# Performance work log

Measured on AMD Instinct MI355X. Metric: run time of the kernel, lower is better.

The kernel has to match this reference:

```python
import jax, jax.numpy as jnp
import numpy as np

DIM = 199  # number of graph nodes, hardcoded in the source repo
K_HOP = 3


def _khop_support(n, k):
    # Ring graph adjacency with self loops, then k-hop reachability mask.
    A = np.eye(n, dtype=np.float64)
    idx = np.arange(n)
    A[idx, (idx + 1) % n] = 1.0
    A[(idx + 1) % n, idx] = 1.0
    S = np.linalg.matrix_power(A, k)
    return (S > 0).astype(np.float32)


def setup_inputs() -> dict:
    key = jax.random.key(0)
    kx, kk = jax.random.split(key)
    batch, n, f = 256, DIM, 1024
    x = jax.random.normal(kx, (batch, n, f), dtype=jnp.float32)
    support = jnp.asarray(_khop_support(n, K_HOP))
    # glorot-uniform-ish kernel
    limit = float(np.sqrt(6.0 / (n + n)))
    kernel = jax.random.uniform(kk, (n, n), minval=-limit, maxval=limit, dtype=jnp.float32)
    bias = jnp.zeros((f,), dtype=jnp.float32)
    return {"x": x, "support": support, "kernel": kernel, "bias": bias}


def reference(x, support, kernel, bias):
    # W = k-hop mask * trainable kernel  -> masked dense matmul over nodes
    W = support * kernel  # [N, N]
    # out[b,m,f] = sum_n x[b,n,f] * W[n,m]  (permute-dot-permute in the original)
    out = jnp.einsum('bnf,nm->bmf', x, W)
    out = out + bias  # broadcast over feature dim
    return out  # activation=None -> linear
```

## Files before the change

### kernel.cpp

```cpp
#include <hip/hip_runtime.h>
#include <stdint.h>


#define CPB 4

__global__ void build_csc_kernel(const float* __restrict__ support,
                                 const float* __restrict__ kern,
                                 int* __restrict__ cnt,
                                 int* __restrict__ idx,
                                 float* __restrict__ val,
                                 int n) {
    const int m = blockIdx.x;
    const int lane = threadIdx.x;
    int base = 0;
    for (int n0 = 0; n0 < n; n0 += 64) {
        const int row = n0 + lane;
        float w = 0.0f;
        if (row < n) w = support[(size_t)row * n + m] * kern[(size_t)row * n + m];
        const unsigned long long mask = __ballot(w != 0.0f);
        const int pos = base + (int)__popcll(mask & ((1ull << lane) - 1ull));
        if (w != 0.0f) {
            idx[(size_t)m * n + pos] = row;
            val[(size_t)m * n + pos] = w;
        }
        base += (int)__popcll(mask);
    }
    if (lane == 0) cnt[m] = base;
}

__global__ void build_band_kernel(const float* __restrict__ support,
                                  const float* __restrict__ kern,
                                  const int* __restrict__ cnt,
                                  float* __restrict__ wband,
                                  int* __restrict__ fastok,
                                  int n) {
    const int m = blockIdx.x * blockDim.x + threadIdx.x;
    if (m >= n) return;
    int cb = 0;
    for (int j = 0; j < 7; ++j) {
        int r = m - 3 + j;
        if (r < 0) r += n;
        if (r >= n) r -= n;
        const float w = support[(size_t)r * n + m] * kern[(size_t)r * n + m];
        wband[(size_t)m * 8 + j] = w;
        cb += (w != 0.0f) ? 1 : 0;
    }
    wband[(size_t)m * 8 + 7] = 0.0f;
    fastok[m] = (n >= 7 && cb == cnt[m] && m >= 3 && m <= n - 4) ? 1 : 0;
}

__global__ __launch_bounds__(256) void spmm_band4_kernel(
    const float4* __restrict__ x, const float* __restrict__ bias,
    const int* __restrict__ cnt, const int* __restrict__ idx,
    const float* __restrict__ val, const float* __restrict__ wband,
    const int* __restrict__ fastok, float4* __restrict__ out,
    int n, int f4, int ngroups, int swizzle) {
    const int blk = blockIdx.x;
    int b, g;
    if (swizzle) {
        const int xcd = blk & 7;
        const int ii = blk >> 3;
        g = ii % ngroups;
        b = xcd + 8 * (ii / ngroups);
    } else {
        b = blk / ngroups;
        g = blk % ngroups;
    }
    const int m0 = g * CPB;
    const float4* __restrict__ xb = x + (size_t)b * n * f4;
    float4* __restrict__ ob = out + (size_t)b * n * f4;
    const float4* __restrict__ b4 = (const float4*)bias;

    for (int t = threadIdx.x; t < f4; t += 256) {
        const float4 bias4 = b4[t];
        float4 win[CPB + 6];
#pragma unroll
        for (int j = 0; j < CPB + 6; ++j) {
            int r = m0 - 3 + j;
            r = (r < 0) ? 0 : ((r >= n) ? (n - 1) : r);
            win[j] = xb[(size_t)r * f4 + t];
        }
#pragma unroll
        for (int dm = 0; dm < CPB; ++dm) {
            const int m = m0 + dm;
            if (m >= n) break;
            float4 a = bias4;
            if (fastok[m]) {
                const float* __restrict__ wb = wband + (size_t)m * 8;
#pragma unroll
                for (int j = 0; j < 7; ++j) {
                    const float w = wb[j];
                    a.x = fmaf(w, win[dm + j].x, a.x);
                    a.y = fmaf(w, win[dm + j].y, a.y);
                    a.z = fmaf(w, win[dm + j].z, a.z);
                    a.w = fmaf(w, win[dm + j].w, a.w);
                }
            } else {
                const int c = cnt[m];
                const int* __restrict__ ip = idx + (size_t)m * n;
                const float* __restrict__ vp = val + (size_t)m * n;
                for (int j = 0; j < c; ++j) {
                    const int nn = ip[j];
                    const float w = vp[j];
                    const float4 v = xb[(size_t)nn * f4 + t];
                    a.x = fmaf(w, v.x, a.x);
                    a.y = fmaf(w, v.y, a.y);
                    a.z = fmaf(w, v.z, a.z);
                    a.w = fmaf(w, v.w, a.w);
                }
            }
            ob[(size_t)m * f4 + t] = a;
        }
    }
}

__global__ __launch_bounds__(256) void dense_fallback_kernel(
    const float4* __restrict__ x, const float* __restrict__ support,
    const float* __restrict__ kern, const float* __restrict__ bias,
    float4* __restrict__ out, int n, int f4) {
    const int blk = blockIdx.x;
    const int b = blk / n;
    const int m = blk % n;
    const float4* __restrict__ b4 = (const float4*)bias;
    const size_t xbase = (size_t)b * n * f4;
    const size_t obase = ((size_t)b * n + m) * f4;
    for (int t = threadIdx.x; t < f4; t += 256) {
        float4 acc = b4[t];
        for (int nn = 0; nn < n; ++nn) {
            const float w = support[(size_t)nn * n + m] * kern[(size_t)nn * n + m];
            if (w != 0.0f) {
                const float4 v = x[xbase + (size_t)nn * f4 + t];
                acc.x = fmaf(w, v.x, acc.x);
                acc.y = fmaf(w, v.y, acc.y);
                acc.z = fmaf(w, v.z, acc.z);
                acc.w = fmaf(w, v.w, acc.w);
            }
        }
        out[obase + t] = acc;
    }
}

extern "C" void kernel_launch(void* const* d_in, const int* in_sizes, int n_in,
                              void* d_out, int out_size, void* d_ws, size_t ws_size,
                              hipStream_t stream) {
    const float* x       = (const float*)d_in[0];
    const float* support = (const float*)d_in[1];
    const float* kern    = (const float*)d_in[2];
    const float* bias    = (const float*)d_in[3];
    float* out = (float*)d_out;

    const int nsq = in_sizes[1];
    int n = 1;
    while (n * n < nsq) ++n;
    const int f = in_sizes[3];
    const int f4 = f / 4;
    const int batch = in_sizes[0] / (n * f);

    const size_t need = ((size_t)2 * n * n + 10u * (size_t)n) * 4u;
    if (ws_size >= need && (f % 4) == 0 && n >= 7) {
        int* cnt = (int*)d_ws;
        int* idx = cnt + n;
        float* val = (float*)(idx + (size_t)n * n);
        float* wband = val + (size_t)n * n;
        int* fastok = (int*)(wband + (size_t)8 * n);
        build_csc_kernel<<<n, 64, 0, stream>>>(support, kern, cnt, idx, val, n);
        build_band_kernel<<<(n + 255) / 256, 256, 0, stream>>>(
            support, kern, cnt, wband, fastok, n);
        const int ngroups = (n + CPB - 1) / CPB;
        const int swz = (batch % 8 == 0) ? 1 : 0;
        spmm_band4_kernel<<<batch * ngroups, 256, 0, stream>>>(
            (const float4*)x, bias, cnt, idx, val, wband, fastok,
            (float4*)out, n, f4, ngroups, swz);
    } else {
        dense_fallback_kernel<<<batch * n, 256, 0, stream>>>(
            (const float4*)x, support, kern, bias, (float4*)out, n, f / 4);
    }
}
```

Measured before the change: 354.5 us.

## Fold band weight construction into the SpMM kernel and drop workspace prepasses

Removes the separate CSC and band-building kernels. Each block now computes its own 7-tap band weights in shared memory, scans its columns of the support and kernel to decide whether the band fast path is valid, and builds a dense weight column in dynamic shared memory for columns that need the general path. This cuts two extra kernel launches and the workspace traffic. In exchange, every one of the many blocks redundantly re-reads strided support and kernel data and adds barriers before streaming x, which could cost more than the launches saved.

```diff
diff --git a/kernel.cpp b/kernel.cpp
--- a/kernel.cpp
+++ b/kernel.cpp
@@ -4,57 +4,15 @@
 
 #define CPB 4
 
-__global__ void build_csc_kernel(const float* __restrict__ support,
-                                 const float* __restrict__ kern,
-                                 int* __restrict__ cnt,
-                                 int* __restrict__ idx,
-                                 float* __restrict__ val,
-                                 int n) {
-    const int m = blockIdx.x;
-    const int lane = threadIdx.x;
-    int base = 0;
-    for (int n0 = 0; n0 < n; n0 += 64) {
-        const int row = n0 + lane;
-        float w = 0.0f;
-        if (row < n) w = support[(size_t)row * n + m] * kern[(size_t)row * n + m];
-        const unsigned long long mask = __ballot(w != 0.0f);
-        const int pos = base + (int)__popcll(mask & ((1ull << lane) - 1ull));
-        if (w != 0.0f) {
-            idx[(size_t)m * n + pos] = row;
-            val[(size_t)m * n + pos] = w;
-        }
-        base += (int)__popcll(mask);
-    }
-    if (lane == 0) cnt[m] = base;
-}
+__global__ __launch_bounds__(256) void spmm_band_nows(
+    const float4* __restrict__ x, const float* __restrict__ support,
+    const float* __restrict__ kern, const float* __restrict__ bias,
+    float4* __restrict__ out, int n, int f4, int ngroups, int swizzle) {
+    extern __shared__ float s_dyn[];
+    __shared__ float s_w[CPB][8];
+    __shared__ int s_ok[CPB];
+    __shared__ int s_any_bad;
 
-__global__ void build_band_kernel(const float* __restrict__ support,
-                                  const float* __restrict__ kern,
-                                  const int* __restrict__ cnt,
-                                  float* __restrict__ wband,
-                                  int* __restrict__ fastok,
-                                  int n) {
-    const int m = blockIdx.x * blockDim.x + threadIdx.x;
-    if (m >= n) return;
-    int cb = 0;
-    for (int j = 0; j < 7; ++j) {
-        int r = m - 3 + j;
-        if (r < 0) r += n;
-        if (r >= n) r -= n;
-        const float w = support[(size_t)r * n + m] * kern[(size_t)r * n + m];
-        wband[(size_t)m * 8 + j] = w;
-        cb += (w != 0.0f) ? 1 : 0;
-    }
-    wband[(size_t)m * 8 + 7] = 0.0f;
-    fastok[m] = (n >= 7 && cb == cnt[m] && m >= 3 && m <= n - 4) ? 1 : 0;
-}
-
-__global__ __launch_bounds__(256) void spmm_band4_kernel(
-    const float4* __restrict__ x, const float* __restrict__ bias,
-    const int* __restrict__ cnt, const int* __restrict__ idx,
-    const float* __restrict__ val, const float* __restrict__ wband,
-    const int* __restrict__ fastok, float4* __restrict__ out,
-    int n, int f4, int ngroups, int swizzle) {
     const int blk = blockIdx.x;
     int b, g;
     if (swizzle) {
@@ -67,11 +25,57 @@
         g = blk % ngroups;
     }
     const int m0 = g * CPB;
+    const int tid = threadIdx.x;
+
+    if (tid < CPB * 7) {
+        const int dm = tid / 7, j = tid % 7;
+        const int m = m0 + dm;
+        float w = 0.0f;
+        if (m < n) {
+            const int r = m - 3 + j;
+            if (r >= 0 && r < n)
+                w = support[(size_t)r * n + m] * kern[(size_t)r * n + m];
+        }
+        s_w[dm][j] = w;
+    }
+    if (tid < CPB) s_ok[tid] = 1;
+    if (tid == 0) s_any_bad = 0;
+    __syncthreads();
+
+#pragma unroll
+    for (int dm = 0; dm < CPB; ++dm) {
+        const int m = m0 + dm;
+        if (m >= n) continue;
+        for (int r = tid; r < n; r += 256) {
+            if (r < m - 3 || r > m + 3) {
+                const float sv = support[(size_t)r * n + m];
+                if (sv != 0.0f && sv * kern[(size_t)r * n + m] != 0.0f) {
+                    s_ok[dm] = 0;
+                    s_any_bad = 1;
+                }
+            }
+        }
+    }
+    __syncthreads();
+
+    if (s_any_bad) {
+#pragma unroll
+        for (int dm = 0; dm < CPB; ++dm) {
+            const int m = m0 + dm;
+            if (m >= n || s_ok[dm]) continue;
+            for (int r = tid; r < n; r += 256)
+                s_dyn[dm * n + r] =
+                    support[(size_t)r * n + m] * kern[(size_t)r * n + m];
+        }
+        __syncthreads();
+    }
+
     const float4* __restrict__ xb = x + (size_t)b * n * f4;
     float4* __restrict__ ob = out + (size_t)b * n * f4;
     const float4* __restrict__ b4 = (const float4*)bias;
+    const int mlim = (n - m0 < CPB) ? (n - m0) : CPB;
 
-    for (int t = threadIdx.x; t < f4; t += 256) {
+    for (int t = tid; t < f4; t += 256) {
         const float4 bias4 = b4[t];
         float4 win[CPB + 6];
 #pragma unroll
@@ -82,31 +86,29 @@
         }
 #pragma unroll
         for (int dm = 0; dm < CPB; ++dm) {
+            if (dm >= mlim) break;
             const int m = m0 + dm;
-            if (m >= n) break;
             float4 a = bias4;
-            if (fastok[m]) {
-                const float* __restrict__ wb = wband + (size_t)m * 8;
+            if (s_ok[dm]) {
 #pragma unroll
                 for (int j = 0; j < 7; ++j) {
-                    const float w = wb[j];
+                    const float w = s_w[dm][j];
                     a.x = fmaf(w, win[dm + j].x, a.x);
                     a.y = fmaf(w, win[dm + j].y, a.y);
                     a.z = fmaf(w, win[dm + j].z, a.z);
                     a.w = fmaf(w, win[dm + j].w, a.w);
                 }
             } else {
-                const int c = cnt[m];
-                const int* __restrict__ ip = idx + (size_t)m * n;
-                const float* __restrict__ vp = val + (size_t)m * n;
-                for (int j = 0; j < c; ++j) {
-                    const int nn = ip[j];
-                    const float w = vp[j];
-                    const float4 v = xb[(size_t)nn * f4 + t];
-                    a.x = fmaf(w, v.x, a.x);
-                    a.y = fmaf(w, v.y, a.y);
-                    a.z = fmaf(w, v.z, a.z);
-                    a.w = fmaf(w, v.w, a.w);
+                const float* __restrict__ wc = s_dyn + dm * n;
+                for (int r = 0; r < n; ++r) {
+                    const float w = wc[r];
+                    if (w != 0.0f) {
+                        const float4 v = xb[(size_t)r * f4 + t];
+                        a.x = fmaf(w, v.x, a.x);
+                        a.y = fmaf(w, v.y, a.y);
+                        a.z = fmaf(w, v.z, a.z);
+                        a.w = fmaf(w, v.w, a.w);
+                    }
                 }
             }
             ob[(size_t)m * f4 + t] = a;
@@ -140,6 +142,25 @@
     }
 }
 
+__global__ __launch_bounds__(256) void dense_scalar_fallback_kernel(
+    const float* __restrict__ x, const float* __restrict__ support,
+    const float* __restrict__ kern, const float* __restrict__ bias,
+    float* __restrict__ out, int n, int f) {
+    const int blk = blockIdx.x;
+    const int b = blk / n;
+    const int m = blk % n;
+    const size_t xbase = (size_t)b * n * f;
+    const size_t obase = ((size_t)b * n + m) * f;
+    for (int t = threadIdx.x; t < f; t += 256) {
+        float acc = bias[t];
+        for (int nn = 0; nn < n; ++nn) {
+            const float w = support[(size_t)nn * n + m] * kern[(size_t)nn * n + m];
+            if (w != 0.0f) acc = fmaf(w, x[xbase + (size_t)nn * f + t], acc);
+        }
+        out[obase + t] = acc;
+    }
+}
+
 extern "C" void kernel_launch(void* const* d_in, const int* in_sizes, int n_in,
                               void* d_out, int out_size, void* d_ws, size_t ws_size,
                               hipStream_t stream) {
@@ -148,31 +169,29 @@
     const float* kern    = (const float*)d_in[2];
     const float* bias    = (const float*)d_in[3];
     float* out = (float*)d_out;
+    (void)d_ws; (void)ws_size;
 
     const int nsq = in_sizes[1];
     int n = 1;
     while (n * n < nsq) ++n;
     const int f = in_sizes[3];
-    const int f4 = f / 4;
     const int batch = in_sizes[0] / (n * f);
 
-    const size_t need = ((size_t)2 * n * n + 10u * (size_t)n) * 4u;
-    if (ws_size >= need && (f % 4) == 0 && n >= 7) {
-        int* cnt = (int*)d_ws;
-        int* idx = cnt + n;
-        float* val = (float*)(idx + (size_t)n * n);
-        float* wband = val + (size_t)n * n;
-        int* fastok = (int*)(wband + (size_t)8 * n);
-        build_csc_kernel<<<n, 64, 0, stream>>>(support, kern, cnt, idx, val, n);
-        build_band_kernel<<<(n + 255) / 256, 256, 0, stream>>>(
-            support, kern, cnt, wband, fastok, n);
-        const int ngroups = (n + CPB - 1) / CPB;
-        const int swz = (batch % 8 == 0) ? 1 : 0;
-        spmm_band4_kernel<<<batch * ngroups, 256, 0, stream>>>(
-            (const float4*)x, bias, cnt, idx, val, wband, fastok,
-            (float4*)out, n, f4, ngroups, swz);
+    if ((f % 4) == 0) {
+        const int f4 = f / 4;
+        const size_t dyn_lds = (size_t)CPB * n * sizeof(float);
+        if (dyn_lds <= 64 * 1024 && n >= 7) {
+            const int ngroups = (n + CPB - 1) / CPB;
+            const int swz = (batch % 8 == 0) ? 1 : 0;
+            spmm_band_nows<<<batch * ngroups, 256, dyn_lds, stream>>>(
+                (const float4*)x, support, kern, bias, (float4*)out,
+                n, f4, ngroups, swz);
+        } else {
+            dense_fallback_kernel<<<batch * n, 256, 0, stream>>>(
+                (const float4*)x, support, kern, bias, (float4*)out, n, f4);
+        }
     } else {
-        dense_fallback_kernel<<<batch * n, 256, 0, stream>>>(
-            (const float4*)x, support, kern, bias, (float4*)out, n, f / 4);
+        dense_scalar_fallback_kernel<<<batch * n, 256, 0, stream>>>(
+            x, support, kern, bias, out, n, f);
     }
 }
```

Result: slower. 402.7 us (+13.6%).
